# Optimization experiments

Measured on AMD Instinct MI355X. Metric: run time of the kernel, lower is better.

Reference implementation:

```python
import jax, jax.numpy as jnp
import numpy as np

L, B, T, D, H = 10, 2, 2040, 256, 4
HD = D // H
TPB = 17  # tokens_per_block (IRIS: 16 obs tokens + 1 action)


def _ln(x, g, b, eps=1e-5):
    mu = x.mean(-1, keepdims=True)
    var = x.var(-1, keepdims=True)
    return (x - mu) / jnp.sqrt(var + eps) * g + b


def _block_causal_mask(t):
    i = jnp.arange(t)[:, None]
    j = jnp.arange(t)[None, :]
    # max(tril(ones), block_diag(ones(TPB,TPB))) == causal OR same-block
    return (j <= i) | ((i // TPB) == (j // TPB))


def setup_inputs() -> dict:
    key = jax.random.key(0)
    ks = jax.random.split(key, 8)
    s = 0.02
    rn = lambda k, shape: jax.random.normal(k, shape, dtype=jnp.float32) * s
    inp = {"sequences": jax.random.normal(ks[0], (B, T, D), dtype=jnp.float32)}
    inp["ln1_g"] = jnp.ones((L, D), jnp.float32); inp["ln1_b"] = jnp.zeros((L, D), jnp.float32)
    inp["wq"] = rn(ks[1], (L, D, D)); inp["bq"] = jnp.zeros((L, D), jnp.float32)
    inp["wk"] = rn(ks[2], (L, D, D)); inp["bk"] = jnp.zeros((L, D), jnp.float32)
    inp["wv"] = rn(ks[3], (L, D, D)); inp["bv"] = jnp.zeros((L, D), jnp.float32)
    inp["wproj"] = rn(ks[4], (L, D, D)); inp["bproj"] = jnp.zeros((L, D), jnp.float32)
    inp["ln2_g"] = jnp.ones((L, D), jnp.float32); inp["ln2_b"] = jnp.zeros((L, D), jnp.float32)
    inp["w1"] = rn(ks[5], (L, D, 4 * D)); inp["b1"] = jnp.zeros((L, 4 * D), jnp.float32)
    inp["w2"] = rn(ks[6], (L, 4 * D, D)); inp["b2"] = jnp.zeros((L, D), jnp.float32)
    inp["lnf_g"] = jnp.ones((D,), jnp.float32); inp["lnf_b"] = jnp.zeros((D,), jnp.float32)
    return inp


def reference(sequences, ln1_g, ln1_b, wq, bq, wk, bk, wv, bv, wproj, bproj,
              ln2_g, ln2_b, w1, b1, w2, b2, lnf_g, lnf_b):
    b, t, d = sequences.shape
    mask = _block_causal_mask(t)
    scale = 1.0 / np.sqrt(HD).astype(np.float32)

    def layer(x, p):
        g1, be1, Wq, Bq, Wk, Bk, Wv, Bv, Wp, Bp, g2, be2, W1, B1, W2, B2 = p
        h = _ln(x, g1, be1)
        def heads(w, bias):
            return (h @ w + bias).reshape(b, t, H, HD).transpose(0, 2, 1, 3)  # bhtd
        q, k, v = heads(Wq, Bq), heads(Wk, Bk), heads(Wv, Bv)
        att = jnp.einsum('bhqd,bhkd->bhqk', q, k) * scale
        att = jax.nn.softmax(jnp.where(mask, att, -jnp.inf), axis=-1)
        y = jnp.einsum('bhqk,bhkd->bhqd', att, v).transpose(0, 2, 1, 3).reshape(b, t, d)
        x = x + y @ Wp + Bp
        h2 = _ln(x, g2, be2)
        x = x + jax.nn.gelu(h2 @ W1 + B1, approximate=False) @ W2 + B2
        return x, None

    params = (ln1_g, ln1_b, wq, bq, wk, bk, wv, bv, wproj, bproj,
              ln2_g, ln2_b, w1, b1, w2, b2)
    x, _ = jax.lax.scan(layer, sequences, params)
    return _ln(x, lnf_g, lnf_b)
```

## Files before the change

kernel.cpp:

```cpp
#include <hip/hip_runtime.h>
#include <math.h>

#define NL 10
#define BSZ 2
#define TSEQ 2040
#define TPAD 2048
#define DMOD 256
#define NH 4
#define HDIM 64
#define DFF 1024
#define MPAD (BSZ*TPAD)
#define CKV 512

typedef __attribute__((ext_vector_type(8))) short bf16x8;
typedef __attribute__((ext_vector_type(4))) short bf16x4;
typedef __attribute__((ext_vector_type(4))) float f32x4;

__device__ __forceinline__ ushort f2b(float f){
  union { float f; unsigned u; } v; v.f = f;
  unsigned u = v.u;
  return (ushort)((u + 0x7FFFu + ((u >> 16) & 1u)) >> 16);
}
__device__ __forceinline__ float b2f(ushort h){
  union { unsigned u; float f; } v; v.u = ((unsigned)h) << 16; return v.f;
}

__global__ __launch_bounds__(256) void copy_in_k(const float* __restrict__ seq, float* __restrict__ x,
                                                 float* __restrict__ pstat){
  int idx = blockIdx.x * 256 + threadIdx.x;
  int row = idx >> 6, c = idx & 63;
  int b = row >> 11, t = row & 2047;
  float4 v = {0.f, 0.f, 0.f, 0.f};
  if (t < TSEQ) v = ((const float4*)(seq + ((size_t)(b * TSEQ + t)) * DMOD))[c];
  ((float4*)(x + (size_t)row * DMOD))[c] = v;
  float s  = v.x + v.y + v.z + v.w;
  float s2 = v.x*v.x + v.y*v.y + v.z*v.z + v.w*v.w;
  #pragma unroll
  for (int off = 1; off < 16; off <<= 1){ s += __shfl_xor(s, off); s2 += __shfl_xor(s2, off); }
  if ((c & 15) == 0){
    float2 pr; pr.x = s; pr.y = s2;
    ((float2*)pstat)[(size_t)row * 4 + (c >> 4)] = pr;
  }
}

__global__ __launch_bounds__(256) void wtrans_k(const float* __restrict__ src, ushort* __restrict__ dst,
                                                int N, int K, int NTOT, int row0){
  __shared__ ushort tile[64][72];
  int tid = threadIdx.x;
  int kk0 = blockIdx.x * 64, n0 = blockIdx.y * 64, l = blockIdx.z;
  int kl = tid >> 2, nq = tid & 3;
  const float* sp = src + ((size_t)(l * K + kk0 + kl)) * N + n0 + nq * 16;
  #pragma unroll
  for (int i = 0; i < 4; ++i){
    float4 v = ((const float4*)sp)[i];
    int nb = nq * 16 + i * 4;
    tile[nb + 0][kl] = f2b(v.x);
    tile[nb + 1][kl] = f2b(v.y);
    tile[nb + 2][kl] = f2b(v.z);
    tile[nb + 3][kl] = f2b(v.w);
  }
  __syncthreads();
  int r = tid >> 2, cq = (tid & 3) * 16;
  ushort* dp = dst + ((size_t)(l * NTOT + row0 + n0 + r)) * K + kk0 + cq;
  *(bf16x8*)dp       = *(const bf16x8*)&tile[r][cq];
  *(bf16x8*)(dp + 8) = *(const bf16x8*)&tile[r][cq + 8];
}

__global__ __launch_bounds__(256) void bqkv_k(const float* __restrict__ bq, const float* __restrict__ bk,
                                              const float* __restrict__ bv, float* __restrict__ bqkv){
  int idx = blockIdx.x * 256 + threadIdx.x;
  if (idx >= NL * 768) return;
  int l = idx / 768, n = idx % 768;
  float v = (n < 256) ? bq[l * 256 + n] : ((n < 512) ? bk[l * 256 + n - 256] : bv[l * 256 + n - 512]);
  bqkv[idx] = v;
}

__global__ __launch_bounds__(256) void lnf_k(const float* __restrict__ x, const float* __restrict__ g,
                                             const float* __restrict__ be, float* __restrict__ outf){
  int tid = threadIdx.x;
  int row = blockIdx.x * 4 + (tid >> 6), lane = tid & 63;
  int b = row / TSEQ, t = row % TSEQ;
  int irow = b * TPAD + t;
  float4 xv = ((const float4*)(x + (size_t)irow * DMOD))[lane];
  float s  = xv.x + xv.y + xv.z + xv.w;
  float s2 = xv.x*xv.x + xv.y*xv.y + xv.z*xv.z + xv.w*xv.w;
  #pragma unroll
  for (int off = 1; off < 64; off <<= 1){ s += __shfl_xor(s, off); s2 += __shfl_xor(s2, off); }
  float mu = s * (1.f/256.f);
  float var = s2 * (1.f/256.f) - mu * mu;
  float rs = rsqrtf(var + 1e-5f);
  float4 gv = ((const float4*)g)[lane];
  float4 bv = ((const float4*)be)[lane];
  float4 ov;
  ov.x = (xv.x - mu) * rs * gv.x + bv.x;
  ov.y = (xv.y - mu) * rs * gv.y + bv.y;
  ov.z = (xv.z - mu) * rs * gv.z + bv.z;
  ov.w = (xv.w - mu) * rs * gv.w + bv.w;
  ((float4*)(outf + (size_t)row * DMOD))[lane] = ov;
}

template<int N, int K, int AMODE, int EPI, int STATS>
__global__ __launch_bounds__(256) void gemm_k(
    const ushort* __restrict__ Ab, const float* __restrict__ Af,
    const float* __restrict__ pstat_in, const float* __restrict__ lng, const float* __restrict__ lnb,
    const ushort* __restrict__ po, const float* __restrict__ pml,
    const ushort* __restrict__ Bt, const float* __restrict__ bias,
    float* __restrict__ xres, float* __restrict__ pstat_out,
    ushort* __restrict__ o0, ushort* __restrict__ o1, ushort* __restrict__ o2){
  __shared__ ushort Alds[2][64][72];
  __shared__ ushort Blds[2][64][72];
  __shared__ float statLds[STATS ? 64 : 1][2][2];
  int tid = threadIdx.x;
  int w = tid >> 6, lane = tid & 63;
  int wr = w >> 1, wc = w & 1;
  int l15 = lane & 15, l4 = lane >> 4;
  int row0 = blockIdx.x * 64, col0 = blockIdx.y * 64;
  int r = tid >> 3, c8 = (tid & 7) * 8;

  float muA = 0.f, rsA = 0.f, muB = 0.f, rsB = 0.f;
  if (AMODE == 1){
    const float4* pa = (const float4*)(pstat_in + (size_t)(row0 + r) * 8);
    float4 a0 = pa[0], a1 = pa[1];
    float s = a0.x + a0.z + a1.x + a1.z, q = a0.y + a0.w + a1.y + a1.w;
    muA = s * (1.f/256.f);
    rsA = rsqrtf(q * (1.f/256.f) - muA * muA + 1e-5f);
    const float4* pb = (const float4*)(pstat_in + (size_t)(row0 + r + 32) * 8);
    float4 b0 = pb[0], b1 = pb[1];
    s = b0.x + b0.z + b1.x + b1.z; q = b0.y + b0.w + b1.y + b1.w;
    muB = s * (1.f/256.f);
    rsB = rsqrtf(q * (1.f/256.f) - muB * muB + 1e-5f);
  }

  f32x4 zero = {0.f, 0.f, 0.f, 0.f};
  f32x4 acc[2][2];
  acc[0][0] = zero; acc[0][1] = zero; acc[1][0] = zero; acc[1][1] = zero;

  for (int k0 = 0; k0 < K; k0 += 128){
    #pragma unroll
    for (int ck = 0; ck < 2; ++ck){
      int kk = k0 + ck * 64;
      #pragma unroll
      for (int it = 0; it < 2; ++it){
        int rr = r + it * 32;
        if (AMODE == 0){
          *(bf16x8*)&Alds[ck][rr][c8] = *(const bf16x8*)(Ab + (size_t)(row0 + rr) * K + kk + c8);
        } else if (AMODE == 1){
          float mu = it ? muB : muA, rs = it ? rsB : rsA;
          const float4* xp = (const float4*)(Af + (size_t)(row0 + rr) * 256 + kk + c8);
          float4 xa = xp[0], xb = xp[1];
          const float4* gp = (const float4*)(lng + kk + c8);
          const float4* bp = (const float4*)(lnb + kk + c8);
          float4 ga = gp[0], gb = gp[1], ba = bp[0], bb = bp[1];
          bf16x8 pk;
          pk[0] = (short)f2b((xa.x - mu) * rs * ga.x + ba.x);
          pk[1] = (short)f2b((xa.y - mu) * rs * ga.y + ba.y);
          pk[2] = (short)f2b((xa.z - mu) * rs * ga.z + ba.z);
          pk[3] = (short)f2b((xa.w - mu) * rs * ga.w + ba.w);
          pk[4] = (short)f2b((xb.x - mu) * rs * gb.x + bb.x);
          pk[5] = (short)f2b((xb.y - mu) * rs * gb.y + bb.y);
          pk[6] = (short)f2b((xb.z - mu) * rs * gb.z + bb.z);
          pk[7] = (short)f2b((xb.w - mu) * rs * gb.w + bb.w);
          *(bf16x8*)&Alds[ck][rr][c8] = pk;
        } else {
          int m = row0 + rr;
          int t = m & 2047, b_ = m >> 11;
          int qt = t >> 4, r16 = t & 15;
          int hh = kk >> 6;
          int u0 = (((b_ * NH + hh) << 7) + qt) << 2;
          int je = ((qt * 16 + 15) / 17) * 17 + 17; je = je < TSEQ ? je : TSEQ;
          int nch = (je + CKV - 1) >> 9;
          float mm[4]; float mg = -1e30f;
          #pragma unroll
          for (int ch = 0; ch < 4; ++ch){
            mm[ch] = (ch < nch) ? pml[(size_t)(u0 + ch) * 32 + r16 * 2] : -1e30f;
            mg = fmaxf(mg, mm[ch]);
          }
          float aw[4]; float lg = 0.f;
          #pragma unroll
          for (int ch = 0; ch < 4; ++ch){
            float ll = (ch < nch) ? pml[(size_t)(u0 + ch) * 32 + r16 * 2 + 1] : 0.f;
            aw[ch] = (ch < nch) ? __expf(mm[ch] - mg) : 0.f;
            lg += aw[ch] * ll;
          }
          float inv = 1.f / lg;
          float av[8] = {0.f,0.f,0.f,0.f,0.f,0.f,0.f,0.f};
          #pragma unroll
          for (int ch = 0; ch < 4; ++ch){
            bf16x8 pv = *(const bf16x8*)(po + (size_t)(u0 + ch) * 1024 + r16 * 64 + c8);
            #pragma unroll
            for (int j = 0; j < 8; ++j) av[j] += aw[ch] * b2f((ushort)pv[j]);
          }
          bf16x8 pk;
          #pragma unroll
          for (int j = 0; j < 8; ++j) pk[j] = (short)f2b(av[j] * inv);
          *(bf16x8*)&Alds[ck][rr][c8] = pk;
        }
        *(bf16x8*)&Blds[ck][rr][c8] = *(const bf16x8*)(Bt + (size_t)(col0 + rr) * K + kk + c8);
      }
    }
    __syncthreads();
    #pragma unroll
    for (int ck = 0; ck < 2; ++ck){
      #pragma unroll
      for (int ks = 0; ks < 2; ++ks){
        bf16x8 af[2], bfr[2];
        #pragma unroll
        for (int i = 0; i < 2; ++i){
          af[i]  = *(const bf16x8*)&Alds[ck][wr * 32 + i * 16 + l15][ks * 32 + l4 * 8];
          bfr[i] = *(const bf16x8*)&Blds[ck][wc * 32 + i * 16 + l15][ks * 32 + l4 * 8];
        }
        #pragma unroll
        for (int mr = 0; mr < 2; ++mr)
          #pragma unroll
          for (int nc = 0; nc < 2; ++nc)
            acc[mr][nc] = __builtin_amdgcn_mfma_f32_16x16x32_bf16(af[mr], bfr[nc], acc[mr][nc], 0, 0, 0);
      }
    }
    __syncthreads();
  }

  float sr_[2][4], q2_[2][4];
  if (STATS){
    #pragma unroll
    for (int mr = 0; mr < 2; ++mr)
      #pragma unroll
      for (int rr = 0; rr < 4; ++rr){ sr_[mr][rr] = 0.f; q2_[mr][rr] = 0.f; }
  }
  #pragma unroll
  for (int mr = 0; mr < 2; ++mr){
    #pragma unroll
    for (int nc = 0; nc < 2; ++nc){
      #pragma unroll
      for (int rr = 0; rr < 4; ++rr){
        int m = row0 + wr * 32 + mr * 16 + l4 * 4 + rr;
        int n = col0 + wc * 32 + nc * 16 + l15;
        float v = acc[mr][nc][rr] + bias[n];
        if (EPI == 0){
          int b = m >> 11, t = m & 2047;
          int which = n >> 8, hn = n & 255, hh = hn >> 6, hd = hn & 63;
          if (which == 0)      o0[(((size_t)(b * NH + hh)) * TPAD + t) * HDIM + hd] = f2b(v * 0.125f);
          else if (which == 1) o1[(((size_t)(b * NH + hh)) * TPAD + t) * HDIM + hd] = f2b(v);
          else                 o2[(((size_t)(b * NH + hh)) * HDIM + hd) * TPAD + t] = f2b(v);
        } else if (EPI == 1){
          float xn = xres[(size_t)m * 256 + n] + v;
          xres[(size_t)m * 256 + n] = xn;
          if (STATS){ sr_[mr][rr] += xn; q2_[mr][rr] += xn * xn; }
        } else {
          float uu = 0.7978845608028654f * (v + 0.044715f * v * v * v);
          float e = __expf(2.f * uu);
          float th = 1.f - 2.f / (e + 1.f);
          o0[(size_t)m * N + n] = f2b(0.5f * v * (1.f + th));
        }
      }
    }
  }
  if (STATS){
    #pragma unroll
    for (int mr = 0; mr < 2; ++mr){
      #pragma unroll
      for (int rr = 0; rr < 4; ++rr){
        float s = sr_[mr][rr], q = q2_[mr][rr];
        #pragma unroll
        for (int off = 1; off < 16; off <<= 1){ s += __shfl_xor(s, off); q += __shfl_xor(q, off); }
        if (l15 == 0){
          int rl = wr * 32 + mr * 16 + l4 * 4 + rr;
          statLds[rl][wc][0] = s;
          statLds[rl][wc][1] = q;
        }
      }
    }
    __syncthreads();
    if (tid < 64){
      float2 pr;
      pr.x = statLds[tid][0][0] + statLds[tid][1][0];
      pr.y = statLds[tid][0][1] + statLds[tid][1][1];
      ((float2*)pstat_out)[(size_t)(row0 + tid) * 4 + blockIdx.y] = pr;
    }
  }
}

__global__ __launch_bounds__(256) void attn_tile_k(const ushort* __restrict__ qq, const ushort* __restrict__ kkk,
                                                   const ushort* __restrict__ vt,
                                                   ushort* __restrict__ po, float* __restrict__ pml){
  __shared__ ushort Klds[64][72];
  __shared__ ushort Vlds[64][72];
  __shared__ ushort Plds[4][16][72];
  int tid = threadIdx.x, w = tid >> 6, lane = tid & 63;
  int l15 = lane & 15, l4 = lane >> 4;
  int qg = blockIdx.x, ch = blockIdx.y, bh = blockIdx.z;
  int r0 = qg * 64;
  int je_blk = ((r0 + 63) / 17 + 1) * 17; je_blk = je_blk < TSEQ ? je_blk : TSEQ;
  int jstart = ch * CKV;
  if (jstart >= je_blk) return;
  int jend = (jstart + CKV) < je_blk ? (jstart + CKV) : je_blk;

  int i0 = r0 + w * 16;
  int je_w = ((i0 + 15) / 17 + 1) * 17; je_w = je_w < TSEQ ? je_w : TSEQ;

  const ushort* qb = qq  + (size_t)bh * TPAD * HDIM;
  const ushort* kb = kkk + (size_t)bh * TPAD * HDIM;
  const ushort* vb = vt  + (size_t)bh * HDIM * TPAD;

  int ig = i0 + l15;
  int ibase = (int)((unsigned)ig / 17u) * 17;
  bf16x8 aq0 = *(const bf16x8*)(qb + (size_t)ig * HDIM + l4 * 8);
  bf16x8 aq1 = *(const bf16x8*)(qb + (size_t)ig * HDIM + 32 + l4 * 8);

  f32x4 zero = {0.f, 0.f, 0.f, 0.f};
  float m_ = -1e30f, l_ = 0.f;
  f32x4 o_[4];
  o_[0] = zero; o_[1] = zero; o_[2] = zero; o_[3] = zero;

  int sr = tid >> 2, sc = (tid & 3) * 16;
  for (int j0 = jstart; j0 < jend; j0 += 64){
    __syncthreads();
    *(bf16x8*)&Klds[sr][sc]     = *(const bf16x8*)(kb + (size_t)(j0 + sr) * HDIM + sc);
    *(bf16x8*)&Klds[sr][sc + 8] = *(const bf16x8*)(kb + (size_t)(j0 + sr) * HDIM + sc + 8);
    *(bf16x8*)&Vlds[sr][sc]     = *(const bf16x8*)(vb + (size_t)sr * TPAD + j0 + sc);
    *(bf16x8*)&Vlds[sr][sc + 8] = *(const bf16x8*)(vb + (size_t)sr * TPAD + j0 + sc + 8);
    __syncthreads();
    if (j0 >= je_w) continue;
    f32x4 s[4];
    #pragma unroll
    for (int f = 0; f < 4; ++f){
      bf16x8 kf = *(const bf16x8*)&Klds[f * 16 + l15][l4 * 8];
      s[f] = __builtin_amdgcn_mfma_f32_16x16x32_bf16(kf, aq0, zero, 0, 0, 0);
    }
    #pragma unroll
    for (int f = 0; f < 4; ++f){
      bf16x8 kf = *(const bf16x8*)&Klds[f * 16 + l15][32 + l4 * 8];
      s[f] = __builtin_amdgcn_mfma_f32_16x16x32_bf16(kf, aq1, s[f], 0, 0, 0);
    }
    if (j0 + 63 > i0){
      #pragma unroll
      for (int f = 0; f < 4; ++f){
        #pragma unroll
        for (int rr = 0; rr < 4; ++rr){
          int jg = j0 + f * 16 + l4 * 4 + rr;
          bool ok = (jg <= ig) || ((unsigned)(jg - ibase) < 17u);
          s[f][rr] = ok ? s[f][rr] : -1e30f;
        }
      }
    }
    float mf0 = fmaxf(fmaxf(s[0][0], s[0][1]), fmaxf(s[0][2], s[0][3]));
    float mf1 = fmaxf(fmaxf(s[1][0], s[1][1]), fmaxf(s[1][2], s[1][3]));
    float mf2 = fmaxf(fmaxf(s[2][0], s[2][1]), fmaxf(s[2][2], s[2][3]));
    float mf3 = fmaxf(fmaxf(s[3][0], s[3][1]), fmaxf(s[3][2], s[3][3]));
    float mx = fmaxf(fmaxf(mf0, mf1), fmaxf(mf2, mf3));
    mx = fmaxf(mx, __shfl_xor(mx, 16));
    mx = fmaxf(mx, __shfl_xor(mx, 32));
    float mn = fmaxf(m_, mx);
    float alpha = __expf(m_ - mn);
    float ps = 0.f;
    #pragma unroll
    for (int f = 0; f < 4; ++f){
      bf16x4 pk;
      #pragma unroll
      for (int rr = 0; rr < 4; ++rr){
        float p = __expf(s[f][rr] - mn);
        ps += p;
        pk[rr] = (short)f2b(p);
      }
      *(bf16x4*)&Plds[w][l15][f * 16 + l4 * 4] = pk;
    }
    ps += __shfl_xor(ps, 16);
    ps += __shfl_xor(ps, 32);
    l_ = l_ * alpha + ps;
    m_ = mn;
    #pragma unroll
    for (int f = 0; f < 4; ++f) o_[f] *= alpha;
    #pragma unroll
    for (int ks = 0; ks < 2; ++ks){
      bf16x8 pf = *(const bf16x8*)&Plds[w][l15][ks * 32 + l4 * 8];
      #pragma unroll
      for (int f = 0; f < 4; ++f){
        bf16x8 vf = *(const bf16x8*)&Vlds[f * 16 + l15][ks * 32 + l4 * 8];
        o_[f] = __builtin_amdgcn_mfma_f32_16x16x32_bf16(vf, pf, o_[f], 0, 0, 0);
      }
    }
  }
  int qt = qg * 4 + w;
  int u = ((bh << 7) + qt) * 4 + ch;
  size_t ob = (size_t)u * 1024;
  #pragma unroll
  for (int f = 0; f < 4; ++f){
    bf16x4 pk;
    #pragma unroll
    for (int rr = 0; rr < 4; ++rr) pk[rr] = (short)f2b(o_[f][rr]);
    *(bf16x4*)&po[ob + (size_t)l15 * 64 + f * 16 + l4 * 4] = pk;
  }
  if (l4 == 0){
    pml[(size_t)u * 32 + l15 * 2 + 0] = m_;
    pml[(size_t)u * 32 + l15 * 2 + 1] = l_;
  }
}

extern "C" void kernel_launch(void* const* d_in, const int* in_sizes, int n_in,
                              void* d_out, int out_size, void* d_ws, size_t ws_size,
                              hipStream_t stream){
  const float* seq    = (const float*)d_in[0];
  const float* ln1_g  = (const float*)d_in[1];
  const float* ln1_b  = (const float*)d_in[2];
  const float* wq     = (const float*)d_in[3];
  const float* bq     = (const float*)d_in[4];
  const float* wk     = (const float*)d_in[5];
  const float* bk     = (const float*)d_in[6];
  const float* wv     = (const float*)d_in[7];
  const float* bv     = (const float*)d_in[8];
  const float* wproj  = (const float*)d_in[9];
  const float* bproj  = (const float*)d_in[10];
  const float* ln2_g  = (const float*)d_in[11];
  const float* ln2_b  = (const float*)d_in[12];
  const float* w1     = (const float*)d_in[13];
  const float* b1     = (const float*)d_in[14];
  const float* w2     = (const float*)d_in[15];
  const float* b2     = (const float*)d_in[16];
  const float* lnf_g  = (const float*)d_in[17];
  const float* lnf_b  = (const float*)d_in[18];

  size_t off = 0;
  char* base = (char*)d_ws;
  auto carve = [&](size_t bytes) -> void* {
    void* p = base + off;
    off += (bytes + 255) & ~(size_t)255;
    return p;
  };
  float*  x      = (float*) carve((size_t)MPAD * DMOD * 4);
  ushort* qbuf   = (ushort*)carve((size_t)BSZ * NH * TPAD * HDIM * 2);
  ushort* kbuf   = (ushort*)carve((size_t)BSZ * NH * TPAD * HDIM * 2);
  ushort* vtbuf  = (ushort*)carve((size_t)BSZ * NH * TPAD * HDIM * 2);
  ushort* mid    = (ushort*)carve((size_t)MPAD * DFF * 2);
  ushort* wqkvT  = (ushort*)carve((size_t)NL * 768 * 256 * 2);
  ushort* wprojT = (ushort*)carve((size_t)NL * 256 * 256 * 2);
  ushort* w1T    = (ushort*)carve((size_t)NL * 1024 * 256 * 2);
  ushort* w2T    = (ushort*)carve((size_t)NL * 256 * 1024 * 2);
  float*  bqkv   = (float*) carve((size_t)NL * 768 * 4);
  ushort* po     = (ushort*)carve((size_t)4096 * 1024 * 2);
  float*  pml    = (float*) carve((size_t)4096 * 32 * 4);
  float*  pstatA = (float*) carve((size_t)MPAD * 8 * 4);
  float*  pstatB = (float*) carve((size_t)MPAD * 8 * 4);
  if (off > ws_size) return;

  copy_in_k<<<dim3(MPAD/4), dim3(256), 0, stream>>>(seq, x, pstatA);
  wtrans_k<<<dim3(4, 4, NL),  dim3(256), 0, stream>>>(wq,    wqkvT,  256, 256,  768, 0);
  wtrans_k<<<dim3(4, 4, NL),  dim3(256), 0, stream>>>(wk,    wqkvT,  256, 256,  768, 256);
  wtrans_k<<<dim3(4, 4, NL),  dim3(256), 0, stream>>>(wv,    wqkvT,  256, 256,  768, 512);
  wtrans_k<<<dim3(4, 4, NL),  dim3(256), 0, stream>>>(wproj, wprojT, 256, 256,  256, 0);
  wtrans_k<<<dim3(4, 16, NL), dim3(256), 0, stream>>>(w1,    w1T,   1024, 256, 1024, 0);
  wtrans_k<<<dim3(16, 4, NL), dim3(256), 0, stream>>>(w2,    w2T,    256,1024,  256, 0);
  bqkv_k<<<dim3((NL*768 + 255)/256), dim3(256), 0, stream>>>(bq, bk, bv, bqkv);

  for (int l = 0; l < NL; ++l){
    gemm_k<768,256,1,0,0><<<dim3(64,12), dim3(256), 0, stream>>>(
        nullptr, x, pstatA, ln1_g + l*256, ln1_b + l*256, nullptr, nullptr,
        wqkvT + (size_t)l*768*256, bqkv + l*768, nullptr, nullptr, qbuf, kbuf, vtbuf);
    attn_tile_k<<<dim3(32,4,8), dim3(256), 0, stream>>>(qbuf, kbuf, vtbuf, po, pml);
    gemm_k<256,256,2,1,1><<<dim3(64,4), dim3(256), 0, stream>>>(
        nullptr, nullptr, nullptr, nullptr, nullptr, po, pml,
        wprojT + (size_t)l*256*256, bproj + l*256, x, pstatB, nullptr, nullptr, nullptr);
    gemm_k<1024,256,1,2,0><<<dim3(64,16), dim3(256), 0, stream>>>(
        nullptr, x, pstatB, ln2_g + l*256, ln2_b + l*256, nullptr, nullptr,
        w1T + (size_t)l*1024*256, b1 + l*1024, nullptr, nullptr, mid, nullptr, nullptr);
    gemm_k<256,1024,0,1,1><<<dim3(64,4), dim3(256), 0, stream>>>(
        mid, nullptr, nullptr, nullptr, nullptr, nullptr, nullptr,
        w2T + (size_t)l*256*1024, b2 + l*256, x, pstatA, nullptr, nullptr, nullptr);
  }
  lnf_k<<<dim3(BSZ*TSEQ/4), dim3(256), 0, stream>>>(x, lnf_g, lnf_b, (float*)d_out);
}
```

Before: 684.4 us.

## Fuse per-layer kernel sequence into one cooperative persistent megakernel with grid syncs

Replaces the 50 per-layer kernel launches with a single cooperative persistent kernel. It loops over layers and stages, with blocks grid-striding over tiles and grid.sync() between stages. The aim is to remove launch overhead and the idle gaps between stages. In exchange it adds grid-wide barrier costs, reduces per-stage concurrency to the number of resident blocks, and uses a shared-memory union sized for the larger of the two stage layouts. The original multi-launch path is kept as a fallback.

New measurement: 1.183 ms. +72.9%, slower.

```diff
diff --git a/kernel.cpp b/kernel.cpp
--- a/kernel.cpp
+++ b/kernel.cpp
@@ -1,5 +1,8 @@
 #include <hip/hip_runtime.h>
+#include <hip/hip_cooperative_groups.h>
 #include <math.h>
+
+namespace cg = cooperative_groups;
 
 #define NL 10
 #define BSZ 2
@@ -11,6 +14,7 @@
 #define DFF 1024
 #define MPAD (BSZ*TPAD)
 #define CKV 512
+#define NCU 256
 
 typedef __attribute__((ext_vector_type(8))) short bf16x8;
 typedef __attribute__((ext_vector_type(4))) short bf16x4;
@@ -24,6 +28,10 @@
 __device__ __forceinline__ float b2f(ushort h){
   union { unsigned u; float f; } v; v.u = ((unsigned)h) << 16; return v.f;
 }
+
+struct GemmSh { ushort A[2][64][72]; ushort B[2][64][72]; float st[64][2][2]; };
+struct AttnSh { ushort K[64][72]; ushort V[64][72]; ushort P[4][16][72]; };
+union ShU { GemmSh g; AttnSh a; };
 
 __global__ __launch_bounds__(256) void copy_in_k(const float* __restrict__ seq, float* __restrict__ x,
                                                  float* __restrict__ pstat){
@@ -100,21 +108,18 @@
 }
 
 template<int N, int K, int AMODE, int EPI, int STATS>
-__global__ __launch_bounds__(256) void gemm_k(
+__device__ void dev_gemm(int bx, int by, GemmSh& sh,
     const ushort* __restrict__ Ab, const float* __restrict__ Af,
     const float* __restrict__ pstat_in, const float* __restrict__ lng, const float* __restrict__ lnb,
     const ushort* __restrict__ po, const float* __restrict__ pml,
     const ushort* __restrict__ Bt, const float* __restrict__ bias,
     float* __restrict__ xres, float* __restrict__ pstat_out,
     ushort* __restrict__ o0, ushort* __restrict__ o1, ushort* __restrict__ o2){
-  __shared__ ushort Alds[2][64][72];
-  __shared__ ushort Blds[2][64][72];
-  __shared__ float statLds[STATS ? 64 : 1][2][2];
   int tid = threadIdx.x;
   int w = tid >> 6, lane = tid & 63;
   int wr = w >> 1, wc = w & 1;
   int l15 = lane & 15, l4 = lane >> 4;
-  int row0 = blockIdx.x * 64, col0 = blockIdx.y * 64;
+  int row0 = bx * 64, col0 = by * 64;
   int r = tid >> 3, c8 = (tid & 7) * 8;
 
   float muA = 0.f, rsA = 0.f, muB = 0.f, rsB = 0.f;
@@ -143,7 +148,7 @@
       for (int it = 0; it < 2; ++it){
         int rr = r + it * 32;
         if (AMODE == 0){
-          *(bf16x8*)&Alds[ck][rr][c8] = *(const bf16x8*)(Ab + (size_t)(row0 + rr) * K + kk + c8);
+          *(bf16x8*)&sh.A[ck][rr][c8] = *(const bf16x8*)(Ab + (size_t)(row0 + rr) * K + kk + c8);
         } else if (AMODE == 1){
           float mu = it ? muB : muA, rs = it ? rsB : rsA;
           const float4* xp = (const float4*)(Af + (size_t)(row0 + rr) * 256 + kk + c8);
@@ -160,7 +165,7 @@
           pk[5] = (short)f2b((xb.y - mu) * rs * gb.y + bb.y);
           pk[6] = (short)f2b((xb.z - mu) * rs * gb.z + bb.z);
           pk[7] = (short)f2b((xb.w - mu) * rs * gb.w + bb.w);
-          *(bf16x8*)&Alds[ck][rr][c8] = pk;
+          *(bf16x8*)&sh.A[ck][rr][c8] = pk;
         } else {
           int m = row0 + rr;
           int t = m & 2047, b_ = m >> 11;
@@ -193,9 +198,9 @@
           bf16x8 pk;
           #pragma unroll
           for (int j = 0; j < 8; ++j) pk[j] = (short)f2b(av[j] * inv);
-          *(bf16x8*)&Alds[ck][rr][c8] = pk;
+          *(bf16x8*)&sh.A[ck][rr][c8] = pk;
         }
-        *(bf16x8*)&Blds[ck][rr][c8] = *(const bf16x8*)(Bt + (size_t)(col0 + rr) * K + kk + c8);
+        *(bf16x8*)&sh.B[ck][rr][c8] = *(const bf16x8*)(Bt + (size_t)(col0 + rr) * K + kk + c8);
       }
     }
     __syncthreads();
@@ -206,8 +211,8 @@
         bf16x8 af[2], bfr[2];
         #pragma unroll
         for (int i = 0; i < 2; ++i){
-          af[i]  = *(const bf16x8*)&Alds[ck][wr * 32 + i * 16 + l15][ks * 32 + l4 * 8];
-          bfr[i] = *(const bf16x8*)&Blds[ck][wc * 32 + i * 16 + l15][ks * 32 + l4 * 8];
+          af[i]  = *(const bf16x8*)&sh.A[ck][wr * 32 + i * 16 + l15][ks * 32 + l4 * 8];
+          bfr[i] = *(const bf16x8*)&sh.B[ck][wc * 32 + i * 16 + l15][ks * 32 + l4 * 8];
         }
         #pragma unroll
         for (int mr = 0; mr < 2; ++mr)
@@ -264,30 +269,28 @@
         for (int off = 1; off < 16; off <<= 1){ s += __shfl_xor(s, off); q += __shfl_xor(q, off); }
         if (l15 == 0){
           int rl = wr * 32 + mr * 16 + l4 * 4 + rr;
-          statLds[rl][wc][0] = s;
-          statLds[rl][wc][1] = q;
+          sh.st[rl][wc][0] = s;
+          sh.st[rl][wc][1] = q;
         }
       }
     }
     __syncthreads();
     if (tid < 64){
       float2 pr;
-      pr.x = statLds[tid][0][0] + statLds[tid][1][0];
-      pr.y = statLds[tid][0][1] + statLds[tid][1][1];
-      ((float2*)pstat_out)[(size_t)(row0 + tid) * 4 + blockIdx.y] = pr;
-    }
-  }
-}
-
-__global__ __launch_bounds__(256) void attn_tile_k(const ushort* __restrict__ qq, const ushort* __restrict__ kkk,
-                                                   const ushort* __restrict__ vt,
-                                                   ushort* __restrict__ po, float* __restrict__ pml){
-  __shared__ ushort Klds[64][72];
-  __shared__ ushort Vlds[64][72];
-  __shared__ ushort Plds[4][16][72];
+      pr.x = sh.st[tid][0][0] + sh.st[tid][1][0];
+      pr.y = sh.st[tid][0][1] + sh.st[tid][1][1];
+      ((float2*)pstat_out)[(size_t)(row0 + tid) * 4 + by] = pr;
+    }
+    __syncthreads();
+  }
+}
+
+__device__ void dev_attn(int qg, int ch, int bh, AttnSh& sh,
+                         const ushort* __restrict__ qq, const ushort* __restrict__ kkk,
+                         const ushort* __restrict__ vt,
+                         ushort* __restrict__ po, float* __restrict__ pml){
   int tid = threadIdx.x, w = tid >> 6, lane = tid & 63;
   int l15 = lane & 15, l4 = lane >> 4;
-  int qg = blockIdx.x, ch = blockIdx.y, bh = blockIdx.z;
   int r0 = qg * 64;
   int je_blk = ((r0 + 63) / 17 + 1) * 17; je_blk = je_blk < TSEQ ? je_blk : TSEQ;
   int jstart = ch * CKV;
@@ -314,21 +317,21 @@
   int sr = tid >> 2, sc = (tid & 3) * 16;
   for (int j0 = jstart; j0 < jend; j0 += 64){
     __syncthreads();
-    *(bf16x8*)&Klds[sr][sc]     = *(const bf16x8*)(kb + (size_t)(j0 + sr) * HDIM + sc);
-    *(bf16x8*)&Klds[sr][sc + 8] = *(const bf16x8*)(kb + (size_t)(j0 + sr) * HDIM + sc + 8);
-    *(bf16x8*)&Vlds[sr][sc]     = *(const bf16x8*)(vb + (size_t)sr * TPAD + j0 + sc);
-    *(bf16x8*)&Vlds[sr][sc + 8] = *(const bf16x8*)(vb + (size_t)sr * TPAD + j0 + sc + 8);
+    *(bf16x8*)&sh.K[sr][sc]     = *(const bf16x8*)(kb + (size_t)(j0 + sr) * HDIM + sc);
+    *(bf16x8*)&sh.K[sr][sc + 8] = *(const bf16x8*)(kb + (size_t)(j0 + sr) * HDIM + sc + 8);
+    *(bf16x8*)&sh.V[sr][sc]     = *(const bf16x8*)(vb + (size_t)sr * TPAD + j0 + sc);
+    *(bf16x8*)&sh.V[sr][sc + 8] = *(const bf16x8*)(vb + (size_t)sr * TPAD + j0 + sc + 8);
     __syncthreads();
     if (j0 >= je_w) continue;
     f32x4 s[4];
     #pragma unroll
     for (int f = 0; f < 4; ++f){
-      bf16x8 kf = *(const bf16x8*)&Klds[f * 16 + l15][l4 * 8];
+      bf16x8 kf = *(const bf16x8*)&sh.K[f * 16 + l15][l4 * 8];
       s[f] = __builtin_amdgcn_mfma_f32_16x16x32_bf16(kf, aq0, zero, 0, 0, 0);
     }
     #pragma unroll
     for (int f = 0; f < 4; ++f){
-      bf16x8 kf = *(const bf16x8*)&Klds[f * 16 + l15][32 + l4 * 8];
+      bf16x8 kf = *(const bf16x8*)&sh.K[f * 16 + l15][32 + l4 * 8];
       s[f] = __builtin_amdgcn_mfma_f32_16x16x32_bf16(kf, aq1, s[f], 0, 0, 0);
     }
     if (j0 + 63 > i0){
@@ -361,7 +364,7 @@
         ps += p;
         pk[rr] = (short)f2b(p);
       }
-      *(bf16x4*)&Plds[w][l15][f * 16 + l4 * 4] = pk;
+      *(bf16x4*)&sh.P[w][l15][f * 16 + l4 * 4] = pk;
     }
     ps += __shfl_xor(ps, 16);
     ps += __shfl_xor(ps, 32);
@@ -371,10 +374,10 @@
     for (int f = 0; f < 4; ++f) o_[f] *= alpha;
     #pragma unroll
     for (int ks = 0; ks < 2; ++ks){
-      bf16x8 pf = *(const bf16x8*)&Plds[w][l15][ks * 32 + l4 * 8];
+      bf16x8 pf = *(const bf16x8*)&sh.P[w][l15][ks * 32 + l4 * 8];
       #pragma unroll
       for (int f = 0; f < 4; ++f){
-        bf16x8 vf = *(const bf16x8*)&Vlds[f * 16 + l15][ks * 32 + l4 * 8];
+        bf16x8 vf = *(const bf16x8*)&sh.V[f * 16 + l15][ks * 32 + l4 * 8];
         o_[f] = __builtin_amdgcn_mfma_f32_16x16x32_bf16(vf, pf, o_[f], 0, 0, 0);
       }
     }
@@ -392,6 +395,62 @@
   if (l4 == 0){
     pml[(size_t)u * 32 + l15 * 2 + 0] = m_;
     pml[(size_t)u * 32 + l15 * 2 + 1] = l_;
+  }
+}
+
+template<int N, int K, int AMODE, int EPI, int STATS>
+__global__ __launch_bounds__(256) void gemm_k(
+    const ushort* Ab, const float* Af, const float* pstat_in, const float* lng, const float* lnb,
+    const ushort* po, const float* pml, const ushort* Bt, const float* bias,
+    float* xres, float* pstat_out, ushort* o0, ushort* o1, ushort* o2){
+  __shared__ GemmSh sh;
+  dev_gemm<N,K,AMODE,EPI,STATS>(blockIdx.x, blockIdx.y, sh, Ab, Af, pstat_in, lng, lnb,
+                                po, pml, Bt, bias, xres, pstat_out, o0, o1, o2);
+}
+
+__global__ __launch_bounds__(256) void attn_tile_k(const ushort* qq, const ushort* kkk, const ushort* vt,
+                                                   ushort* po, float* pml){
+  __shared__ AttnSh sh;
+  dev_attn(blockIdx.x, blockIdx.y, blockIdx.z, sh, qq, kkk, vt, po, pml);
+}
+
+struct MegaP {
+  float* x; float* pstatA; float* pstatB;
+  ushort *qbuf, *kbuf, *vtbuf, *mid, *po; float* pml;
+  const ushort *wqkvT, *wprojT, *w1T, *w2T;
+  const float *bqkv, *bproj, *b1, *b2;
+  const float *ln1_g, *ln1_b, *ln2_g, *ln2_b;
+};
+
+__global__ __launch_bounds__(256) void mega_k(MegaP p){
+  __shared__ ShU sh;
+  cg::grid_group grid = cg::this_grid();
+  for (int l = 0; l < NL; ++l){
+    for (int bid = blockIdx.x; bid < 768; bid += gridDim.x)
+      dev_gemm<768,256,1,0,0>(bid & 63, bid >> 6, sh.g, nullptr, p.x, p.pstatA,
+                              p.ln1_g + l*256, p.ln1_b + l*256, nullptr, nullptr,
+                              p.wqkvT + (size_t)l*768*256, p.bqkv + l*768,
+                              nullptr, nullptr, p.qbuf, p.kbuf, p.vtbuf);
+    grid.sync();
+    for (int bid = blockIdx.x; bid < 1024; bid += gridDim.x)
+      dev_attn(bid & 31, (bid >> 5) & 3, bid >> 7, sh.a, p.qbuf, p.kbuf, p.vtbuf, p.po, p.pml);
+    grid.sync();
+    for (int bid = blockIdx.x; bid < 256; bid += gridDim.x)
+      dev_gemm<256,256,2,1,1>(bid & 63, bid >> 6, sh.g, nullptr, nullptr, nullptr, nullptr, nullptr,
+                              p.po, p.pml, p.wprojT + (size_t)l*256*256, p.bproj + l*256,
+                              p.x, p.pstatB, nullptr, nullptr, nullptr);
+    grid.sync();
+    for (int bid = blockIdx.x; bid < 1024; bid += gridDim.x)
+      dev_gemm<1024,256,1,2,0>(bid & 63, bid >> 6, sh.g, nullptr, p.x, p.pstatB,
+                               p.ln2_g + l*256, p.ln2_b + l*256, nullptr, nullptr,
+                               p.w1T + (size_t)l*1024*256, p.b1 + l*1024,
+                               nullptr, nullptr, p.mid, nullptr, nullptr);
+    grid.sync();
+    for (int bid = blockIdx.x; bid < 256; bid += gridDim.x)
+      dev_gemm<256,1024,0,1,1>(bid & 63, bid >> 6, sh.g, p.mid, nullptr, nullptr, nullptr, nullptr,
+                               nullptr, nullptr, p.w2T + (size_t)l*256*1024, p.b2 + l*256,
+                               p.x, p.pstatA, nullptr, nullptr, nullptr);
+    grid.sync();
   }
 }
 
@@ -450,20 +509,42 @@
   wtrans_k<<<dim3(16, 4, NL), dim3(256), 0, stream>>>(w2,    w2T,    256,1024,  256, 0);
   bqkv_k<<<dim3((NL*768 + 255)/256), dim3(256), 0, stream>>>(bq, bk, bv, bqkv);
 
-  for (int l = 0; l < NL; ++l){
-    gemm_k<768,256,1,0,0><<<dim3(64,12), dim3(256), 0, stream>>>(
-        nullptr, x, pstatA, ln1_g + l*256, ln1_b + l*256, nullptr, nullptr,
-        wqkvT + (size_t)l*768*256, bqkv + l*768, nullptr, nullptr, qbuf, kbuf, vtbuf);
-    attn_tile_k<<<dim3(32,4,8), dim3(256), 0, stream>>>(qbuf, kbuf, vtbuf, po, pml);
-    gemm_k<256,256,2,1,1><<<dim3(64,4), dim3(256), 0, stream>>>(
-        nullptr, nullptr, nullptr, nullptr, nullptr, po, pml,
-        wprojT + (size_t)l*256*256, bproj + l*256, x, pstatB, nullptr, nullptr, nullptr);
-    gemm_k<1024,256,1,2,0><<<dim3(64,16), dim3(256), 0, stream>>>(
-        nullptr, x, pstatB, ln2_g + l*256, ln2_b + l*256, nullptr, nullptr,
-        w1T + (size_t)l*1024*256, b1 + l*1024, nullptr, nullptr, mid, nullptr, nullptr);
-    gemm_k<256,1024,0,1,1><<<dim3(64,4), dim3(256), 0, stream>>>(
-        mid, nullptr, nullptr, nullptr, nullptr, nullptr, nullptr,
-        w2T + (size_t)l*256*1024, b2 + l*256, x, pstatA, nullptr, nullptr, nullptr);
+  int maxb = 0;
+  hipError_t qe = hipOccupancyMaxActiveBlocksPerMultiprocessor(&maxb, (const void*)mega_k, 256, 0);
+  int nblk = (qe == hipSuccess) ? maxb * NCU : 0;
+  if (nblk > 1024) nblk = 1024;
+
+  bool coop_done = false;
+  if (nblk >= 256){
+    MegaP prm;
+    prm.x = x; prm.pstatA = pstatA; prm.pstatB = pstatB;
+    prm.qbuf = qbuf; prm.kbuf = kbuf; prm.vtbuf = vtbuf; prm.mid = mid;
+    prm.po = po; prm.pml = pml;
+    prm.wqkvT = wqkvT; prm.wprojT = wprojT; prm.w1T = w1T; prm.w2T = w2T;
+    prm.bqkv = bqkv; prm.bproj = bproj; prm.b1 = b1; prm.b2 = b2;
+    prm.ln1_g = ln1_g; prm.ln1_b = ln1_b; prm.ln2_g = ln2_g; prm.ln2_b = ln2_b;
+    void* kargs[] = { (void*)&prm };
+    hipError_t le = hipLaunchCooperativeKernel((const void*)mega_k, dim3(nblk), dim3(256),
+                                               kargs, 0, stream);
+    coop_done = (le == hipSuccess);
+  }
+
+  if (!coop_done){
+    for (int l = 0; l < NL; ++l){
+      gemm_k<768,256,1,0,0><<<dim3(64,12), dim3(256), 0, stream>>>(
+          nullptr, x, pstatA, ln1_g + l*256, ln1_b + l*256, nullptr, nullptr,
+          wqkvT + (size_t)l*768*256, bqkv + l*768, nullptr, nullptr, qbuf, kbuf, vtbuf);
+      attn_tile_k<<<dim3(32,4,8), dim3(256), 0, stream>>>(qbuf, kbuf, vtbuf, po, pml);
+      gemm_k<256,256,2,1,1><<<dim3(64,4), dim3(256), 0, stream>>>(
+          nullptr, nullptr, nullptr, nullptr, nullptr, po, pml,
+          wprojT + (size_t)l*256*256, bproj + l*256, x, pstatB, nullptr, nullptr, nullptr);
+      gemm_k<1024,256,1,2,0><<<dim3(64,16), dim3(256), 0, stream>>>(
+          nullptr, x, pstatB, ln2_g + l*256, ln2_b + l*256, nullptr, nullptr,
+          w1T + (size_t)l*1024*256, b1 + l*1024, nullptr, nullptr, mid, nullptr, nullptr);
+      gemm_k<256,1024,0,1,1><<<dim3(64,4), dim3(256), 0, stream>>>(
+          mid, nullptr, nullptr, nullptr, nullptr, nullptr, nullptr,
+          w2T + (size_t)l*256*1024, b2 + l*256, x, pstatA, nullptr, nullptr, nullptr);
+    }
   }
   lnf_k<<<dim3(BSZ*TSEQ/4), dim3(256), 0, stream>>>(x, lnf_g, lnf_b, (float*)d_out);
 }
```
